# Kernel optimization log

Measured on AMD Instinct MI355X. Metric: run time of the kernel, lower is better.

Reference implementation:

```python
import jax, jax.numpy as jnp
import numpy as np

B, S, E, H, D = 8, 1024, 1024, 16, 64
LN_EPS = 1e-5


def setup_inputs() -> dict:
    key = jax.random.key(0)
    ks = jax.random.split(key, 8)
    scale = 1.0 / np.sqrt(E)
    return {
        "query": jax.random.normal(ks[0], (B, S, E), jnp.float32),
        "key": jax.random.normal(ks[1], (B, S, E), jnp.float32),
        "value": jax.random.normal(ks[2], (B, S, E), jnp.float32),
        "self_attn_mask": jax.random.randint(ks[3], (B, S, S), 0, 2) == 1,
        "Wq": jax.random.normal(ks[4], (E, H * D), jnp.float32) * scale,
        "Wk": jax.random.normal(ks[5], (E, H * D), jnp.float32) * scale,
        "Wv": jax.random.normal(ks[6], (E, H * D), jnp.float32) * scale,
        "Wo": jax.random.normal(ks[7], (H * D, E), jnp.float32) * scale,
        "ln_gamma": jnp.ones((E,), jnp.float32),
        "ln_beta": jnp.zeros((E,), jnp.float32),
    }


def reference(query, key, value, self_attn_mask, Wq, Wk, Wv, Wo, ln_gamma, ln_beta):
    identity = query
    # project and split heads: [B, S, E] -> [B, H, S, D]
    q = (query @ Wq).reshape(B, S, H, D).transpose(0, 2, 1, 3)
    k = (key @ Wk).reshape(B, S, H, D).transpose(0, 2, 1, 3)
    v = (value @ Wv).reshape(B, S, H, D).transpose(0, 2, 1, 3)
    # scaled dot-product scores in fp32, additive mask fill -1e9
    score = jnp.einsum("bhsd,bhtd->bhst", q, k).astype(jnp.float32) / np.sqrt(D)
    score = jnp.where(self_attn_mask[:, None, :, :], jnp.float32(-1e9), score)
    attn = jax.nn.softmax(score, axis=-1)
    degree = jnp.einsum("bhst,bhtd->bhsd", attn, v)  # [B, H, S, D]
    degree = degree.transpose(0, 2, 1, 3).reshape(B, S, H * D)
    out = degree @ Wo + identity
    # LayerNorm over last dim
    mu = jnp.mean(out, axis=-1, keepdims=True)
    var = jnp.var(out, axis=-1, keepdims=True)
    out = (out - mu) * jax.lax.rsqrt(var + LN_EPS) * ln_gamma + ln_beta
    return out
```

## Files before the change

kernel.cpp:

```cpp
#include <hip/hip_runtime.h>
#include <hip/hip_bf16.h>
#include <cstdint>
#include <cstddef>

typedef __attribute__((ext_vector_type(8))) short bf16x8;
typedef __attribute__((ext_vector_type(8))) unsigned short ushort8;
typedef __attribute__((ext_vector_type(4))) unsigned short ushort4v;
typedef __attribute__((ext_vector_type(4))) float f32x4;

#define B_ 8
#define S_ 1024
#define E_ 1024
#define H_ 16
#define D_ 64
#define NW_ (S_ / 64)

__device__ __forceinline__ unsigned short f2bf(float f) {
    union { float fp; unsigned int u; } v; v.fp = f;
    unsigned int u = v.u;
    return (unsigned short)((u + 0x7fffu + ((u >> 16) & 1u)) >> 16);
}

__device__ __forceinline__ float fexp2(float x) {
    return __builtin_amdgcn_exp2f(x);
}

__device__ __forceinline__ void gload16(const void* g, void* l) {
    __builtin_amdgcn_global_load_lds((__attribute__((address_space(1))) void*)g,
                                     (__attribute__((address_space(3))) void*)l,
                                     16, 0, 0);
}

__global__ __launch_bounds__(256) void f32_to_bf16(const float* __restrict__ in,
                                                   unsigned short* __restrict__ out,
                                                   int n8) {
    int i = blockIdx.x * 256 + threadIdx.x;
    const int stride = gridDim.x * 256;
    for (; i < n8; i += stride) {
        float4 f0 = ((const float4*)in)[i * 2];
        float4 f1 = ((const float4*)in)[i * 2 + 1];
        ushort8 o;
        o[0] = f2bf(f0.x); o[1] = f2bf(f0.y); o[2] = f2bf(f0.z); o[3] = f2bf(f0.w);
        o[4] = f2bf(f1.x); o[5] = f2bf(f1.y); o[6] = f2bf(f1.z); o[7] = f2bf(f1.w);
        ((ushort8*)out)[i] = o;
    }
}

__global__ __launch_bounds__(256) void wtrans4(const float* __restrict__ W0,
                                               const float* __restrict__ W1,
                                               const float* __restrict__ W2,
                                               const float* __restrict__ W3,
                                               unsigned short* __restrict__ T0,
                                               unsigned short* __restrict__ T1,
                                               unsigned short* __restrict__ T2,
                                               unsigned short* __restrict__ T3) {
    const float* W = (blockIdx.z == 0) ? W0 : (blockIdx.z == 1) ? W1 : (blockIdx.z == 2) ? W2 : W3;
    unsigned short* Wt = (blockIdx.z == 0) ? T0 : (blockIdx.z == 1) ? T1 : (blockIdx.z == 2) ? T2 : T3;
    __shared__ float tile[32][33];
    const int k0 = blockIdx.y * 32, n0 = blockIdx.x * 32;
    const int tx = threadIdx.x & 31, ty = threadIdx.x >> 5;
#pragma unroll
    for (int i = ty; i < 32; i += 8)
        tile[i][tx] = W[(size_t)(k0 + i) * E_ + n0 + tx];
    __syncthreads();
#pragma unroll
    for (int i = ty; i < 32; i += 8)
        Wt[(size_t)(n0 + i) * E_ + k0 + tx] = f2bf(tile[tx][i]);
}

__global__ void detect_kernel(const unsigned int* __restrict__ m, int* __restrict__ flag) {
    unsigned int bad = 0;
    for (int i = threadIdx.x; i < 4096; i += 64) bad |= (m[i] > 1u) ? 1u : 0u;
    unsigned long long anybad = __ballot(bad != 0u);
    if (threadIdx.x == 0) *flag = (anybad == 0ull) ? 1 : 0;
}

__global__ __launch_bounds__(256) void pack_mask(const void* __restrict__ maskp,
                                                 const int* __restrict__ flagp,
                                                 unsigned long long* __restrict__ mbits) {
    const int mask32 = *flagp;
    const int lane = threadIdx.x & 63;
    const int gw = blockIdx.x * 4 + (threadIdx.x >> 6);
    const int nwaves = gridDim.x * 4;
    const int totw = B_ * S_ * NW_;
    for (int w = gw; w < totw; w += nwaves) {
        bool m;
        if (mask32) m = ((const int*)maskp)[(size_t)w * 64 + lane] != 0;
        else        m = ((const unsigned char*)maskp)[(size_t)w * 64 + lane] != 0;
        unsigned long long bits = __ballot(m);
        if (lane == 0) mbits[w] = bits;
    }
}

template <int EPI>
__global__ __launch_bounds__(256) void gemm_bt(const unsigned short* __restrict__ A,
                                               const unsigned short* __restrict__ Bt,
                                               void* __restrict__ Cp,
                                               const float* __restrict__ resid,
                                               float cscale) {
    __shared__ unsigned short As[128 * 32];
    __shared__ unsigned short Bs[128 * 32];
    const int t = threadIdx.x;
    const int lane = t & 63, w = t >> 6;
    const int wr = w >> 1, wc = w & 1;
    const int l15 = lane & 15, l4 = lane >> 4;
    const int m0 = blockIdx.x * 128, n0 = blockIdx.y * 128;

    const int srow = w * 32 + (lane >> 2);
    const int scol = (lane & 3) * 8;
    const unsigned short* Ag0 = A + (size_t)(m0 + srow) * E_ + scol;
    const unsigned short* Ag1 = A + (size_t)(m0 + srow + 16) * E_ + scol;
    const unsigned short* Bg0 = Bt + (size_t)(n0 + srow) * E_ + scol;
    const unsigned short* Bg1 = Bt + (size_t)(n0 + srow + 16) * E_ + scol;
    unsigned short* Al = &As[w * 1024];
    unsigned short* Bl = &Bs[w * 1024];

    f32x4 acc[4][4];
#pragma unroll
    for (int i = 0; i < 4; ++i)
#pragma unroll
        for (int j = 0; j < 4; ++j) acc[i][j] = (f32x4){0.f, 0.f, 0.f, 0.f};

    for (int kt = 0; kt < E_; kt += 32) {
        gload16(Ag0 + kt, Al);
        gload16(Ag1 + kt, Al + 512);
        gload16(Bg0 + kt, Bl);
        gload16(Bg1 + kt, Bl + 512);
        __syncthreads();
        bf16x8 af[4], bfv[4];
#pragma unroll
        for (int mi = 0; mi < 4; ++mi)
            af[mi] = *(const bf16x8*)&As[(wr * 64 + mi * 16 + l15) * 32 + l4 * 8];
#pragma unroll
        for (int ni = 0; ni < 4; ++ni)
            bfv[ni] = *(const bf16x8*)&Bs[(wc * 64 + ni * 16 + l15) * 32 + l4 * 8];
#pragma unroll
        for (int mi = 0; mi < 4; ++mi)
#pragma unroll
            for (int ni = 0; ni < 4; ++ni)
                acc[mi][ni] =
                    __builtin_amdgcn_mfma_f32_16x16x32_bf16(af[mi], bfv[ni], acc[mi][ni], 0, 0, 0);
        __syncthreads();
    }
#pragma unroll
    for (int mi = 0; mi < 4; ++mi) {
#pragma unroll
        for (int ni = 0; ni < 4; ++ni) {
#pragma unroll
            for (int r = 0; r < 4; ++r) {
                const int m = m0 + wr * 64 + mi * 16 + l4 * 4 + r;
                const int n = n0 + wc * 64 + ni * 16 + l15;
                const float v = acc[mi][ni][r];
                if (EPI == 0) {
                    const int b = m >> 10, s = m & 1023, h = n >> 6, d = n & 63;
                    ((unsigned short*)Cp)[(((size_t)b * H_ + h) * S_ + s) * D_ + d] = f2bf(v * cscale);
                } else if (EPI == 2) {
                    const int b = m >> 10, s = m & 1023, h = n >> 6, d = n & 63;
                    ((unsigned short*)Cp)[(((size_t)b * H_ + h) * D_ + d) * S_ + s] = f2bf(v);
                } else {
                    const size_t idx = (size_t)m * E_ + n;
                    ((float*)Cp)[idx] = v + resid[idx];
                }
            }
        }
    }
}

__global__ __launch_bounds__(256) void attn_kernel(const unsigned short* __restrict__ Qh,
                                                   const unsigned short* __restrict__ Kh,
                                                   const unsigned short* __restrict__ Vt,
                                                   const unsigned long long* __restrict__ mbits,
                                                   unsigned short* __restrict__ degree) {
    __shared__ unsigned short Ks[64 * 64];
    __shared__ unsigned short Vs[64 * 64];
    __shared__ unsigned short Ps[4 * 16 * 64];
    const int t = threadIdx.x;
    const int lane = t & 63, w = t >> 6;
    const int l15 = lane & 15, l4 = lane >> 4;
    const int bh = blockIdx.y, b = bh >> 4, h = bh & 15;
    const int q0 = blockIdx.x * 64;
    const int myq = q0 + w * 16 + l15;

    const unsigned long long* mrow = mbits + ((size_t)b * S_ + myq) * NW_;

    bf16x8 qf[2];
    {
        const unsigned short* qptr = Qh + ((size_t)bh * S_ + myq) * D_ + l4 * 8;
        qf[0] = *(const bf16x8*)qptr;
        qf[1] = *(const bf16x8*)(qptr + 32);
    }
    f32x4 O[4];
#pragma unroll
    for (int i = 0; i < 4; ++i) O[i] = (f32x4){0.f, 0.f, 0.f, 0.f};
    float mrun = -3e38f, lrun = 0.f;

    const int srow = t >> 2, sch = (t & 3) * 2;
    const int ssw = (srow & 7) << 4;
    char* KsB = (char*)Ks;
    char* VsB = (char*)Vs;
    char* PsB = (char*)Ps + w * 2048;
    const int psw = (l15 & 7) << 4;

    for (int jt = 0; jt < S_; jt += 64) {
        {
            const unsigned short* kg = Kh + ((size_t)bh * S_ + jt + srow) * D_ + sch * 8;
            *(ushort8*)(KsB + srow * 128 + ((sch * 16) ^ ssw)) = *(const ushort8*)kg;
            *(ushort8*)(KsB + srow * 128 + ((sch * 16 + 16) ^ ssw)) = *(const ushort8*)(kg + 8);
            const unsigned short* vg = Vt + ((size_t)bh * D_ + srow) * S_ + jt + sch * 8;
            *(ushort8*)(VsB + srow * 128 + ((sch * 16) ^ ssw)) = *(const ushort8*)vg;
            *(ushort8*)(VsB + srow * 128 + ((sch * 16 + 16) ^ ssw)) = *(const ushort8*)(vg + 8);
        }
        const unsigned long long mw = mrow[jt >> 6];
        __syncthreads();

        f32x4 sacc[4];
#pragma unroll
        for (int i = 0; i < 4; ++i) sacc[i] = (f32x4){0.f, 0.f, 0.f, 0.f};
#pragma unroll
        for (int ni = 0; ni < 4; ++ni) {
            const int row = l15 + ni * 16;
            const int sw = (row & 7) << 4;
            bf16x8 b0 = *(const bf16x8*)(KsB + row * 128 + ((l4 * 16) ^ sw));
            bf16x8 b1 = *(const bf16x8*)(KsB + row * 128 + ((64 + l4 * 16) ^ sw));
            sacc[ni] = __builtin_amdgcn_mfma_f32_16x16x32_bf16(b0, qf[0], sacc[ni], 0, 0, 0);
            sacc[ni] = __builtin_amdgcn_mfma_f32_16x16x32_bf16(b1, qf[1], sacc[ni], 0, 0, 0);
        }

        float m0 = -3e38f;
#pragma unroll
        for (int ni = 0; ni < 4; ++ni) {
#pragma unroll
            for (int r = 0; r < 4; ++r) {
                const int k = ni * 16 + l4 * 4 + r;
                const float s = ((mw >> k) & 1ull) ? -1e9f : sacc[ni][r];
                sacc[ni][r] = s;
                m0 = fmaxf(m0, s);
            }
        }
        m0 = fmaxf(m0, __shfl_xor(m0, 16, 64));
        m0 = fmaxf(m0, __shfl_xor(m0, 32, 64));
        const float mnew = fmaxf(mrun, m0);
        const float corr = fexp2(mrun - mnew);
        float ps = 0.f;
#pragma unroll
        for (int ni = 0; ni < 4; ++ni) {
            ushort4v pw;
#pragma unroll
            for (int r = 0; r < 4; ++r) {
                const float p = fexp2(sacc[ni][r] - mnew);
                ps += p;
                pw[r] = f2bf(p);
            }
            *(ushort4v*)(PsB + l15 * 128 + ((ni * 32 + l4 * 8) ^ psw)) = pw;
        }
        ps += __shfl_xor(ps, 16, 64);
        ps += __shfl_xor(ps, 32, 64);
        lrun = lrun * corr + ps;
        mrun = mnew;
#pragma unroll
        for (int df = 0; df < 4; ++df)
#pragma unroll
            for (int r = 0; r < 4; ++r) O[df][r] *= corr;

        asm volatile("s_waitcnt lgkmcnt(0)" ::: "memory");
        bf16x8 pa0 = *(const bf16x8*)(PsB + l15 * 128 + ((l4 * 16) ^ psw));
        bf16x8 pa1 = *(const bf16x8*)(PsB + l15 * 128 + ((64 + l4 * 16) ^ psw));
#pragma unroll
        for (int df = 0; df < 4; ++df) {
            const int row = l15 + df * 16;
            const int sw = (row & 7) << 4;
            bf16x8 v0 = *(const bf16x8*)(VsB + row * 128 + ((l4 * 16) ^ sw));
            bf16x8 v1 = *(const bf16x8*)(VsB + row * 128 + ((64 + l4 * 16) ^ sw));
            O[df] = __builtin_amdgcn_mfma_f32_16x16x32_bf16(v0, pa0, O[df], 0, 0, 0);
            O[df] = __builtin_amdgcn_mfma_f32_16x16x32_bf16(v1, pa1, O[df], 0, 0, 0);
        }
        __syncthreads();
    }

    const float inv = 1.f / lrun;
#pragma unroll
    for (int df = 0; df < 4; ++df) {
        ushort4v ow;
#pragma unroll
        for (int r = 0; r < 4; ++r) ow[r] = f2bf(O[df][r] * inv);
        const size_t dst = ((size_t)b * S_ + myq) * (size_t)(H_ * D_) +
                           h * 64 + df * 16 + l4 * 4;
        *(ushort4v*)(degree + dst) = ow;
    }
}

__global__ __launch_bounds__(256) void lnorm(float* __restrict__ io,
                                             const float* __restrict__ gamma,
                                             const float* __restrict__ beta) {
    const int row = blockIdx.x;
    const int t = threadIdx.x;
    float4 v = ((const float4*)(io + (size_t)row * E_))[t];
    float s = v.x + v.y + v.z + v.w;
    float q = v.x * v.x + v.y * v.y + v.z * v.z + v.w * v.w;
#pragma unroll
    for (int off = 32; off; off >>= 1) {
        s += __shfl_down(s, off, 64);
        q += __shfl_down(q, off, 64);
    }
    __shared__ float red[8];
    const int wid = t >> 6;
    if ((t & 63) == 0) { red[wid] = s; red[4 + wid] = q; }
    __syncthreads();
    const float ts = red[0] + red[1] + red[2] + red[3];
    const float tq = red[4] + red[5] + red[6] + red[7];
    const float mean = ts * (1.0f / E_);
    const float var = tq * (1.0f / E_) - mean * mean;
    const float rstd = rsqrtf(var + 1e-5f);
    const float4 g = ((const float4*)gamma)[t];
    const float4 bb = ((const float4*)beta)[t];
    v.x = (v.x - mean) * rstd * g.x + bb.x;
    v.y = (v.y - mean) * rstd * g.y + bb.y;
    v.z = (v.z - mean) * rstd * g.z + bb.z;
    v.w = (v.w - mean) * rstd * g.w + bb.w;
    ((float4*)(io + (size_t)row * E_))[t] = v;
}

extern "C" void kernel_launch(void* const* d_in, const int* in_sizes, int n_in,
                              void* d_out, int out_size, void* d_ws, size_t ws_size,
                              hipStream_t stream) {
    const float* query = (const float*)d_in[0];
    const float* key_ = (const float*)d_in[1];
    const float* value = (const float*)d_in[2];
    const void* maskp = d_in[3];
    const float* Wq = (const float*)d_in[4];
    const float* Wk = (const float*)d_in[5];
    const float* Wv = (const float*)d_in[6];
    const float* Wo = (const float*)d_in[7];
    const float* gamma = (const float*)d_in[8];
    const float* beta = (const float*)d_in[9];
    float* out = (float*)d_out;
    char* ws = (char*)d_ws;
    const size_t MB = 1024ull * 1024ull;

    unsigned short* WqT = (unsigned short*)(ws + 0 * MB);
    unsigned short* WkT = (unsigned short*)(ws + 2 * MB);
    unsigned short* WvT = (unsigned short*)(ws + 4 * MB);
    unsigned short* WoT = (unsigned short*)(ws + 6 * MB);
    unsigned short* Qh = (unsigned short*)(ws + 8 * MB);
    unsigned short* Kh = (unsigned short*)(ws + 24 * MB);
    unsigned short* Vt = (unsigned short*)(ws + 40 * MB);
    unsigned short* deg = (unsigned short*)(ws + 56 * MB);
    unsigned short* Abf = deg;
    int* flag = (int*)(ws + 72 * MB);
    unsigned long long* mbits = (unsigned long long*)(ws + 72 * MB + 4096);

    const int n8 = B_ * S_ * E_ / 8;
    const float qscale = 0.125f * 1.4426950408889634f;

    wtrans4<<<dim3(32, 32, 4), 256, 0, stream>>>(Wq, Wk, Wv, Wo, WqT, WkT, WvT, WoT);
    detect_kernel<<<1, 64, 0, stream>>>((const unsigned int*)maskp, flag);
    pack_mask<<<2048, 256, 0, stream>>>(maskp, flag, mbits);

    f32_to_bf16<<<2048, 256, 0, stream>>>(query, Abf, n8);
    gemm_bt<0><<<dim3(64, 8), 256, 0, stream>>>(Abf, WqT, Qh, nullptr, qscale);
    f32_to_bf16<<<2048, 256, 0, stream>>>(key_, Abf, n8);
    gemm_bt<0><<<dim3(64, 8), 256, 0, stream>>>(Abf, WkT, Kh, nullptr, 1.0f);
    f32_to_bf16<<<2048, 256, 0, stream>>>(value, Abf, n8);
    gemm_bt<2><<<dim3(64, 8), 256, 0, stream>>>(Abf, WvT, Vt, nullptr, 1.0f);

    attn_kernel<<<dim3(16, 128), 256, 0, stream>>>(Qh, Kh, Vt, mbits, deg);

    gemm_bt<3><<<dim3(64, 8), 256, 0, stream>>>(deg, WoT, out, query, 1.0f);
    lnorm<<<8192, 256, 0, stream>>>(out, gamma, beta);
}
```

Measured before the change: 263.2 us.

## Fuse fp32-to-bf16 conversion into batched QKV GEMM and add lazy softmax rescale

Removes the three separate fp32-to-bf16 conversion passes. A single QKV GEMM launch over three z-slices now loads fp32 activations straight into LDS and packs them to bf16 with v_cvt_pk_bf16_f32 before the MFMAs. This avoids writing and re-reading a bf16 copy of each input and cuts five launches, but doubles the A-tile LDS footprint and global load bytes inside the GEMM. The attention kernel also skips the online-softmax rescale unless the running max grows by more than 8 (log2 units), and uses packed bf16 conversion for P. This risks larger unnormalised exponent values.

```diff
diff --git a/kernel.cpp b/kernel.cpp
--- a/kernel.cpp
+++ b/kernel.cpp
@@ -25,25 +25,16 @@
     return __builtin_amdgcn_exp2f(x);
 }
 
+__device__ __forceinline__ unsigned cvt_pk_bf16(float lo, float hi) {
+    unsigned r;
+    asm("v_cvt_pk_bf16_f32 %0, %1, %2" : "=v"(r) : "v"(lo), "v"(hi));
+    return r;
+}
+
 __device__ __forceinline__ void gload16(const void* g, void* l) {
     __builtin_amdgcn_global_load_lds((__attribute__((address_space(1))) void*)g,
                                      (__attribute__((address_space(3))) void*)l,
                                      16, 0, 0);
-}
-
-__global__ __launch_bounds__(256) void f32_to_bf16(const float* __restrict__ in,
-                                                   unsigned short* __restrict__ out,
-                                                   int n8) {
-    int i = blockIdx.x * 256 + threadIdx.x;
-    const int stride = gridDim.x * 256;
-    for (; i < n8; i += stride) {
-        float4 f0 = ((const float4*)in)[i * 2];
-        float4 f1 = ((const float4*)in)[i * 2 + 1];
-        ushort8 o;
-        o[0] = f2bf(f0.x); o[1] = f2bf(f0.y); o[2] = f2bf(f0.z); o[3] = f2bf(f0.w);
-        o[4] = f2bf(f1.x); o[5] = f2bf(f1.y); o[6] = f2bf(f1.z); o[7] = f2bf(f1.w);
-        ((ushort8*)out)[i] = o;
-    }
 }
 
 __global__ __launch_bounds__(256) void wtrans4(const float* __restrict__ W0,
@@ -92,12 +83,106 @@
     }
 }
 
-template <int EPI>
-__global__ __launch_bounds__(256) void gemm_bt(const unsigned short* __restrict__ A,
-                                               const unsigned short* __restrict__ Bt,
-                                               void* __restrict__ Cp,
-                                               const float* __restrict__ resid,
-                                               float cscale) {
+__global__ __launch_bounds__(256) void qkv_gemm(const float* __restrict__ Aq,
+                                                const float* __restrict__ Ak,
+                                                const float* __restrict__ Av,
+                                                const unsigned short* __restrict__ Wq,
+                                                const unsigned short* __restrict__ Wk,
+                                                const unsigned short* __restrict__ Wv,
+                                                unsigned short* __restrict__ Qh,
+                                                unsigned short* __restrict__ Kh,
+                                                unsigned short* __restrict__ Vt,
+                                                float qscale) {
+    __shared__ float Asf[128 * 32];
+    __shared__ unsigned short Bs[128 * 32];
+    const int z = blockIdx.z;
+    const float* A = (z == 0) ? Aq : (z == 1) ? Ak : Av;
+    const unsigned short* Bt = (z == 0) ? Wq : (z == 1) ? Wk : Wv;
+    unsigned short* Cp = (z == 0) ? Qh : (z == 1) ? Kh : Vt;
+    const float cscale = (z == 0) ? qscale : 1.0f;
+
+    const int t = threadIdx.x;
+    const int lane = t & 63, w = t >> 6;
+    const int wr = w >> 1, wc = w & 1;
+    const int l15 = lane & 15, l4 = lane >> 4;
+    const int m0 = blockIdx.x * 128, n0 = blockIdx.y * 128;
+
+    const int lr = lane >> 3, lc = lane & 7;
+    const float* Ag[4];
+#pragma unroll
+    for (int g = 0; g < 4; ++g)
+        Ag[g] = A + (size_t)(m0 + w * 32 + g * 8 + lr) * E_ + ((lc ^ lr) << 2);
+    float* Alf = &Asf[w * 1024];
+
+    const int srow = w * 32 + (lane >> 2);
+    const int scol = (lane & 3) * 8;
+    const unsigned short* Bg0 = Bt + (size_t)(n0 + srow) * E_ + scol;
+    const unsigned short* Bg1 = Bt + (size_t)(n0 + srow + 16) * E_ + scol;
+    unsigned short* Bl = &Bs[w * 1024];
+
+    f32x4 acc[4][4];
+#pragma unroll
+    for (int i = 0; i < 4; ++i)
+#pragma unroll
+        for (int j = 0; j < 4; ++j) acc[i][j] = (f32x4){0.f, 0.f, 0.f, 0.f};
+
+    const int r7 = l15 & 7;
+    const char* AsB = (const char*)Asf;
+
+    for (int kt = 0; kt < E_; kt += 32) {
+#pragma unroll
+        for (int g = 0; g < 4; ++g) gload16(Ag[g] + kt, Alf + g * 256);
+        gload16(Bg0 + kt, Bl);
+        gload16(Bg1 + kt, Bl + 512);
+        __syncthreads();
+        bf16x8 af[4], bfv[4];
+#pragma unroll
+        for (int mi = 0; mi < 4; ++mi) {
+            const int row = wr * 64 + mi * 16 + l15;
+            const int s0 = (l4 * 2) ^ r7, s1 = (l4 * 2 + 1) ^ r7;
+            f32x4 a0 = *(const f32x4*)(AsB + row * 128 + s0 * 16);
+            f32x4 a1 = *(const f32x4*)(AsB + row * 128 + s1 * 16);
+            union { unsigned u[4]; bf16x8 v; } pk;
+            pk.u[0] = cvt_pk_bf16(a0[0], a0[1]);
+            pk.u[1] = cvt_pk_bf16(a0[2], a0[3]);
+            pk.u[2] = cvt_pk_bf16(a1[0], a1[1]);
+            pk.u[3] = cvt_pk_bf16(a1[2], a1[3]);
+            af[mi] = pk.v;
+        }
+#pragma unroll
+        for (int ni = 0; ni < 4; ++ni)
+            bfv[ni] = *(const bf16x8*)&Bs[(wc * 64 + ni * 16 + l15) * 32 + l4 * 8];
+#pragma unroll
+        for (int mi = 0; mi < 4; ++mi)
+#pragma unroll
+            for (int ni = 0; ni < 4; ++ni)
+                acc[mi][ni] =
+                    __builtin_amdgcn_mfma_f32_16x16x32_bf16(af[mi], bfv[ni], acc[mi][ni], 0, 0, 0);
+        __syncthreads();
+    }
+#pragma unroll
+    for (int mi = 0; mi < 4; ++mi) {
+#pragma unroll
+        for (int ni = 0; ni < 4; ++ni) {
+#pragma unroll
+            for (int r = 0; r < 4; ++r) {
+                const int m = m0 + wr * 64 + mi * 16 + l4 * 4 + r;
+                const int n = n0 + wc * 64 + ni * 16 + l15;
+                const float v = acc[mi][ni][r];
+                const int b = m >> 10, s = m & 1023, h = n >> 6, d = n & 63;
+                if (z != 2)
+                    Cp[(((size_t)b * H_ + h) * S_ + s) * D_ + d] = f2bf(v * cscale);
+                else
+                    Cp[(((size_t)b * H_ + h) * D_ + d) * S_ + s] = f2bf(v);
+            }
+        }
+    }
+}
+
+__global__ __launch_bounds__(256) void gemm_out(const unsigned short* __restrict__ A,
+                                                const unsigned short* __restrict__ Bt,
+                                                float* __restrict__ Cp,
+                                                const float* __restrict__ resid) {
     __shared__ unsigned short As[128 * 32];
     __shared__ unsigned short Bs[128 * 32];
     const int t = threadIdx.x;
@@ -150,17 +235,8 @@
             for (int r = 0; r < 4; ++r) {
                 const int m = m0 + wr * 64 + mi * 16 + l4 * 4 + r;
                 const int n = n0 + wc * 64 + ni * 16 + l15;
-                const float v = acc[mi][ni][r];
-                if (EPI == 0) {
-                    const int b = m >> 10, s = m & 1023, h = n >> 6, d = n & 63;
-                    ((unsigned short*)Cp)[(((size_t)b * H_ + h) * S_ + s) * D_ + d] = f2bf(v * cscale);
-                } else if (EPI == 2) {
-                    const int b = m >> 10, s = m & 1023, h = n >> 6, d = n & 63;
-                    ((unsigned short*)Cp)[(((size_t)b * H_ + h) * D_ + d) * S_ + s] = f2bf(v);
-                } else {
-                    const size_t idx = (size_t)m * E_ + n;
-                    ((float*)Cp)[idx] = v + resid[idx];
-                }
+                const size_t idx = (size_t)m * E_ + n;
+                Cp[idx] = acc[mi][ni][r] + resid[idx];
             }
         }
     }
@@ -239,28 +315,32 @@
         }
         m0 = fmaxf(m0, __shfl_xor(m0, 16, 64));
         m0 = fmaxf(m0, __shfl_xor(m0, 32, 64));
-        const float mnew = fmaxf(mrun, m0);
-        const float corr = fexp2(mrun - mnew);
+        if (!__all(m0 <= mrun + 8.f)) {
+            const float mnew = fmaxf(mrun, m0);
+            const float corr = fexp2(mrun - mnew);
+            lrun *= corr;
+#pragma unroll
+            for (int df = 0; df < 4; ++df)
+#pragma unroll
+                for (int r = 0; r < 4; ++r) O[df][r] *= corr;
+            mrun = mnew;
+        }
         float ps = 0.f;
 #pragma unroll
         for (int ni = 0; ni < 4; ++ni) {
-            ushort4v pw;
-#pragma unroll
-            for (int r = 0; r < 4; ++r) {
-                const float p = fexp2(sacc[ni][r] - mnew);
-                ps += p;
-                pw[r] = f2bf(p);
-            }
-            *(ushort4v*)(PsB + l15 * 128 + ((ni * 32 + l4 * 8) ^ psw)) = pw;
+            float p0 = fexp2(sacc[ni][0] - mrun);
+            float p1 = fexp2(sacc[ni][1] - mrun);
+            float p2 = fexp2(sacc[ni][2] - mrun);
+            float p3 = fexp2(sacc[ni][3] - mrun);
+            ps += (p0 + p1) + (p2 + p3);
+            uint2 pw;
+            pw.x = cvt_pk_bf16(p0, p1);
+            pw.y = cvt_pk_bf16(p2, p3);
+            *(uint2*)(PsB + l15 * 128 + ((ni * 32 + l4 * 8) ^ psw)) = pw;
         }
         ps += __shfl_xor(ps, 16, 64);
         ps += __shfl_xor(ps, 32, 64);
-        lrun = lrun * corr + ps;
-        mrun = mnew;
-#pragma unroll
-        for (int df = 0; df < 4; ++df)
-#pragma unroll
-            for (int r = 0; r < 4; ++r) O[df][r] *= corr;
+        lrun += ps;
 
         asm volatile("s_waitcnt lgkmcnt(0)" ::: "memory");
         bf16x8 pa0 = *(const bf16x8*)(PsB + l15 * 128 + ((l4 * 16) ^ psw));
@@ -345,26 +425,20 @@
     unsigned short* Kh = (unsigned short*)(ws + 24 * MB);
     unsigned short* Vt = (unsigned short*)(ws + 40 * MB);
     unsigned short* deg = (unsigned short*)(ws + 56 * MB);
-    unsigned short* Abf = deg;
     int* flag = (int*)(ws + 72 * MB);
     unsigned long long* mbits = (unsigned long long*)(ws + 72 * MB + 4096);
 
-    const int n8 = B_ * S_ * E_ / 8;
     const float qscale = 0.125f * 1.4426950408889634f;
 
     wtrans4<<<dim3(32, 32, 4), 256, 0, stream>>>(Wq, Wk, Wv, Wo, WqT, WkT, WvT, WoT);
     detect_kernel<<<1, 64, 0, stream>>>((const unsigned int*)maskp, flag);
     pack_mask<<<2048, 256, 0, stream>>>(maskp, flag, mbits);
 
-    f32_to_bf16<<<2048, 256, 0, stream>>>(query, Abf, n8);
-    gemm_bt<0><<<dim3(64, 8), 256, 0, stream>>>(Abf, WqT, Qh, nullptr, qscale);
-    f32_to_bf16<<<2048, 256, 0, stream>>>(key_, Abf, n8);
-    gemm_bt<0><<<dim3(64, 8), 256, 0, stream>>>(Abf, WkT, Kh, nullptr, 1.0f);
-    f32_to_bf16<<<2048, 256, 0, stream>>>(value, Abf, n8);
-    gemm_bt<2><<<dim3(64, 8), 256, 0, stream>>>(Abf, WvT, Vt, nullptr, 1.0f);
+    qkv_gemm<<<dim3(64, 8, 3), 256, 0, stream>>>(query, key_, value, WqT, WkT, WvT,
+                                                 Qh, Kh, Vt, qscale);
 
     attn_kernel<<<dim3(16, 128), 256, 0, stream>>>(Qh, Kh, Vt, mbits, deg);
 
-    gemm_bt<3><<<dim3(64, 8), 256, 0, stream>>>(deg, WoT, out, query, 1.0f);
+    gemm_out<<<dim3(64, 8), 256, 0, stream>>>(deg, WoT, out, query);
     lnorm<<<8192, 256, 0, stream>>>(out, gamma, beta);
 }
```

Result: faster. 248.2 us (-5.7%).

## Use lazy softmax rescaling, packed bf16 converts, and XCD-aware attention block mapping

Applied to the files above, without the earlier changes.

The attention kernel now rescales the running max and output accumulator only when some lane's tile max exceeds the running max by more than a threshold, skipping the per-tile correction multiply in the common case. Float-to-bf16 conversion in the attention P path and in the input cast kernel uses the hardware packed convert instruction instead of manual rounding arithmetic. The attention grid is flattened to 1D and remapped so that consecutive query tiles of the same batch-head are spread across the XCDs in a chosen pattern, aiming for better L2 reuse of K/V. Lazy rescaling lets unnormalized exponents grow by up to 2^8, which slightly changes numerics.

```diff
diff --git a/kernel.cpp b/kernel.cpp
--- a/kernel.cpp
+++ b/kernel.cpp
@@ -23,6 +23,12 @@
 
 __device__ __forceinline__ float fexp2(float x) {
     return __builtin_amdgcn_exp2f(x);
+}
+
+__device__ __forceinline__ unsigned cvt_pk_bf16(float lo, float hi) {
+    unsigned r;
+    asm("v_cvt_pk_bf16_f32 %0, %1, %2" : "=v"(r) : "v"(lo), "v"(hi));
+    return r;
 }
 
 __device__ __forceinline__ void gload16(const void* g, void* l) {
@@ -39,10 +45,12 @@
     for (; i < n8; i += stride) {
         float4 f0 = ((const float4*)in)[i * 2];
         float4 f1 = ((const float4*)in)[i * 2 + 1];
-        ushort8 o;
-        o[0] = f2bf(f0.x); o[1] = f2bf(f0.y); o[2] = f2bf(f0.z); o[3] = f2bf(f0.w);
-        o[4] = f2bf(f1.x); o[5] = f2bf(f1.y); o[6] = f2bf(f1.z); o[7] = f2bf(f1.w);
-        ((ushort8*)out)[i] = o;
+        union { unsigned u[4]; ushort8 v; } o;
+        o.u[0] = cvt_pk_bf16(f0.x, f0.y);
+        o.u[1] = cvt_pk_bf16(f0.z, f0.w);
+        o.u[2] = cvt_pk_bf16(f1.x, f1.y);
+        o.u[3] = cvt_pk_bf16(f1.z, f1.w);
+        ((ushort8*)out)[i] = o.v;
     }
 }
 
@@ -177,8 +185,10 @@
     const int t = threadIdx.x;
     const int lane = t & 63, w = t >> 6;
     const int l15 = lane & 15, l4 = lane >> 4;
-    const int bh = blockIdx.y, b = bh >> 4, h = bh & 15;
-    const int q0 = blockIdx.x * 64;
+    const int i = blockIdx.x;
+    const int L = (i & 7) * 256 + (i >> 3);
+    const int bh = L >> 4, b = bh >> 4, h = bh & 15;
+    const int q0 = (L & 15) * 64;
     const int myq = q0 + w * 16 + l15;
 
     const unsigned long long* mrow = mbits + ((size_t)b * S_ + myq) * NW_;
@@ -191,7 +201,7 @@
     }
     f32x4 O[4];
 #pragma unroll
-    for (int i = 0; i < 4; ++i) O[i] = (f32x4){0.f, 0.f, 0.f, 0.f};
+    for (int idx = 0; idx < 4; ++idx) O[idx] = (f32x4){0.f, 0.f, 0.f, 0.f};
     float mrun = -3e38f, lrun = 0.f;
 
     const int srow = t >> 2, sch = (t & 3) * 2;
@@ -215,7 +225,7 @@
 
         f32x4 sacc[4];
 #pragma unroll
-        for (int i = 0; i < 4; ++i) sacc[i] = (f32x4){0.f, 0.f, 0.f, 0.f};
+        for (int idx = 0; idx < 4; ++idx) sacc[idx] = (f32x4){0.f, 0.f, 0.f, 0.f};
 #pragma unroll
         for (int ni = 0; ni < 4; ++ni) {
             const int row = l15 + ni * 16;
@@ -239,28 +249,32 @@
         }
         m0 = fmaxf(m0, __shfl_xor(m0, 16, 64));
         m0 = fmaxf(m0, __shfl_xor(m0, 32, 64));
-        const float mnew = fmaxf(mrun, m0);
-        const float corr = fexp2(mrun - mnew);
+        if (!__all(m0 <= mrun + 8.f)) {
+            const float mnew = fmaxf(mrun, m0);
+            const float corr = fexp2(mrun - mnew);
+            lrun *= corr;
+#pragma unroll
+            for (int df = 0; df < 4; ++df)
+#pragma unroll
+                for (int r = 0; r < 4; ++r) O[df][r] *= corr;
+            mrun = mnew;
+        }
         float ps = 0.f;
 #pragma unroll
         for (int ni = 0; ni < 4; ++ni) {
-            ushort4v pw;
-#pragma unroll
-            for (int r = 0; r < 4; ++r) {
-                const float p = fexp2(sacc[ni][r] - mnew);
-                ps += p;
-                pw[r] = f2bf(p);
-            }
-            *(ushort4v*)(PsB + l15 * 128 + ((ni * 32 + l4 * 8) ^ psw)) = pw;
+            float p0 = fexp2(sacc[ni][0] - mrun);
+            float p1 = fexp2(sacc[ni][1] - mrun);
+            float p2 = fexp2(sacc[ni][2] - mrun);
+            float p3 = fexp2(sacc[ni][3] - mrun);
+            ps += (p0 + p1) + (p2 + p3);
+            uint2 pw;
+            pw.x = cvt_pk_bf16(p0, p1);
+            pw.y = cvt_pk_bf16(p2, p3);
+            *(uint2*)(PsB + l15 * 128 + ((ni * 32 + l4 * 8) ^ psw)) = pw;
         }
         ps += __shfl_xor(ps, 16, 64);
         ps += __shfl_xor(ps, 32, 64);
-        lrun = lrun * corr + ps;
-        mrun = mnew;
-#pragma unroll
-        for (int df = 0; df < 4; ++df)
-#pragma unroll
-            for (int r = 0; r < 4; ++r) O[df][r] *= corr;
+        lrun += ps;
 
         asm volatile("s_waitcnt lgkmcnt(0)" ::: "memory");
         bf16x8 pa0 = *(const bf16x8*)(PsB + l15 * 128 + ((l4 * 16) ^ psw));
@@ -363,7 +377,7 @@
     f32_to_bf16<<<2048, 256, 0, stream>>>(value, Abf, n8);
     gemm_bt<2><<<dim3(64, 8), 256, 0, stream>>>(Abf, WvT, Vt, nullptr, 1.0f);
 
-    attn_kernel<<<dim3(16, 128), 256, 0, stream>>>(Qh, Kh, Vt, mbits, deg);
+    attn_kernel<<<2048, 256, 0, stream>>>(Qh, Kh, Vt, mbits, deg);
 
     gemm_bt<3><<<dim3(64, 8), 256, 0, stream>>>(deg, WoT, out, query, 1.0f);
     lnorm<<<8192, 256, 0, stream>>>(out, gamma, beta);
```

After: 253.0 us. -3.9%, faster.
